# Performance work log

Hardware: AMD Instinct MI355X
Metric: run time of the kernel (lower is better)

Reference implementation:

```python
import jax, jax.numpy as jnp
import numpy as np

B, L, H, R = 8, 128, 768, 24


def setup_inputs() -> dict:
    key = jax.random.key(0)
    ks = jax.random.split(key, 12)
    s = 0.02  # init scale
    f32 = jnp.float32
    inp = {
        "embed_tokens": jax.random.normal(ks[0], (B, L, H), f32),
        "attention_mask": jnp.ones((B, L), f32),
        "target_rel": jax.random.randint(ks[1], (B,), 0, R),
        # relation-judgement head
        "W_hr": jax.random.normal(ks[2], (H, H // 2), f32) * s,
        "b_hr": jnp.zeros((H // 2,), f32),
        "W_rj": jax.random.normal(ks[3], (H // 2, R), f32) * s,
        "b_rj": jnp.zeros((R,), f32),
        # relation embedding
        "rel_emb": jax.random.normal(ks[4], (R, H), f32) * s,
        # correspondence matrix head (input is concat -> 2H)
        "W_corr": jax.random.normal(ks[5], (2 * H, H), f32) * s,
        "b_corr": jnp.zeros((H,), f32),
        "W_gc": jax.random.normal(ks[6], (H, 1), f32) * s,
        "b_gc": jnp.zeros((1,), f32),
        # subject tagging head (fusion_type='concat' -> 2H in, H hidden)
        "W_sh": jax.random.normal(ks[7], (2 * H, H), f32) * s,
        "b_sh": jnp.zeros((H,), f32),
        "W_st": jax.random.normal(ks[8], (H, 3), f32) * s,
        "b_st": jnp.zeros((3,), f32),
        # object tagging head
        "W_oh": jax.random.normal(ks[9], (2 * H, H), f32) * s,
        "b_oh": jnp.zeros((H,), f32),
        "W_ot": jax.random.normal(ks[10], (H, 3), f32) * s,
        "b_ot": jnp.zeros((3,), f32),
    }
    return inp


def reference(embed_tokens, attention_mask, target_rel,
              W_hr, b_hr, W_rj, b_rj, rel_emb,
              W_corr, b_corr, W_gc, b_gc,
              W_sh, b_sh, W_st, b_st,
              W_oh, b_oh, W_ot, b_ot):
    # ---- stage 1: masked mean-pool + relation judgement (dropout = identity at inference)
    masked = embed_tokens * attention_mask[:, :, None]            # [B,L,H]
    pool = jnp.sum(masked, axis=1) / jnp.sum(attention_mask, axis=1)[:, None]  # [B,H]
    rel_hidden = jax.nn.relu(pool @ W_hr + b_hr)                  # [B,H/2]
    stage1 = rel_hidden @ W_rj + b_rj                             # [B,R]

    # ---- correspondence matrix: concat[b,i,j] = [embed[b,j], embed[b,i]]
    # Decompose concat-linear: concat @ W_corr = embed_j @ W1 + embed_i @ W2
    W1, W2 = W_corr[:H_dim(embed_tokens)], W_corr[H_dim(embed_tokens):]
    A = embed_tokens @ W1                                         # [B,L,H] (j-index part)
    C = embed_tokens @ W2                                         # [B,L,H] (i-index part)
    corres_hidden = jax.nn.relu(A[:, None, :, :] + C[:, :, None, :] + b_corr)  # [B,L,L,H]
    pred_corres = corres_hidden @ W_gc + b_gc                     # [B,L,L,1]

    # ---- relation-fused tagging (mode == 'train')
    re = rel_emb[target_rel]                                      # [B,H]
    Bsz, Lsz, Hsz = embed_tokens.shape
    fusion = jnp.concatenate(
        [jnp.broadcast_to(re[:, None, :], (Bsz, Lsz, Hsz)), embed_tokens], axis=-1)  # [B,L,2H]
    subj = jax.nn.relu(fusion @ W_sh + b_sh) @ W_st + b_st        # [B,L,3]
    obj = jax.nn.relu(fusion @ W_oh + b_oh) @ W_ot + b_ot         # [B,L,3]

    return stage1, subj, obj, pred_corres


def H_dim(x):
    return x.shape[-1]
```

## Files before the change

kernel.cpp:

```cpp
#include <hip/hip_runtime.h>
#include <hip/hip_bf16.h>

#define BD   8
#define LD   128
#define HD   768
#define RD   24
#define H2D  384
#define NF   1536
#define WSZ  589824

typedef __attribute__((ext_vector_type(8))) short bf16x8;
typedef __attribute__((ext_vector_type(4))) float f32x4;

__device__ __forceinline__ short f2bf(float f) {
    __hip_bfloat16 h = __float2bfloat16(f);
    return *reinterpret_cast<short*>(&h);
}

__device__ __forceinline__ f32x4 vmax0(f32x4 v) {
    f32x4 r;
    r[0] = fmaxf(v[0], 0.f); r[1] = fmaxf(v[1], 0.f);
    r[2] = fmaxf(v[2], 0.f); r[3] = fmaxf(v[3], 0.f);
    return r;
}

__global__ __launch_bounds__(256) void prep_kernel(
        const float* __restrict__ embed, const float* __restrict__ mask,
        const float* __restrict__ rel_emb, const int* __restrict__ trel,
        const float* __restrict__ W_corr,
        const float* __restrict__ W_sh, const float* __restrict__ b_sh,
        const float* __restrict__ W_oh, const float* __restrict__ b_oh,
        const float* __restrict__ b_st, const float* __restrict__ b_ot,
        float* __restrict__ pool, float* __restrict__ biasrel,
        unsigned short* __restrict__ embedB, unsigned short* __restrict__ WT,
        float* __restrict__ out_subj, float* __restrict__ out_obj) {
    const int q = blockIdx.x, tid = threadIdx.x;

    if (q < 96) {
        const int b = q / 12, c = q % 12;
        __shared__ float mrow[LD];
        __shared__ float msum;
        __shared__ float part[4][64];
        if (tid < LD) mrow[tid] = mask[b * LD + tid];
        __syncthreads();
        if (tid == 0) {
            float s = 0.f;
            for (int l = 0; l < LD; ++l) s += mrow[l];
            msum = s;
        }
        __syncthreads();
        const int lc = tid >> 6, hh = tid & 63;
        const int h = c * 64 + hh;
        float acc = 0.f;
        const float* base = embed + ((size_t)b * LD + lc * 32) * HD + h;
#pragma unroll 8
        for (int i = 0; i < 32; ++i) acc += base[(size_t)i * HD] * mrow[lc * 32 + i];
        part[lc][hh] = acc;
        __syncthreads();
        if (lc == 0)
            pool[b * HD + h] = (part[0][hh] + part[1][hh] + part[2][hh] + part[3][hh]) / msum;
    } else if (q < 192) {
        const int qq = q - 96;
        const int b = qq / 12, cc = qq % 12;
        __shared__ float re[HD];
        __shared__ float part2[2][128];
        const int rel = trel[b];
        for (int k = tid; k < HD; k += 256) re[k] = rel_emb[(size_t)rel * HD + k];
        if (cc == 0 && tid < 3 * LD) {
            const int l = tid / 3, t = tid - 3 * l;
            out_subj[(b * LD + l) * 3 + t] = b_st[t];
            out_obj [(b * LD + l) * 3 + t] = b_ot[t];
        }
        __syncthreads();
        const int kc = tid >> 7, nn = tid & 127;
        const int n = cc * 128 + nn;
        const float* Wp; float bb; int col;
        if (n < HD) { Wp = W_sh; bb = b_sh[n];      col = n; }
        else        { Wp = W_oh; bb = b_oh[n - HD]; col = n - HD; }
        float acc = 0.f;
#pragma unroll 8
        for (int i = 0; i < 384; ++i) {
            const int k = kc * 384 + i;
            acc += re[k] * Wp[(size_t)k * HD + col];
        }
        part2[kc][nn] = acc;
        __syncthreads();
        if (kc == 0) biasrel[b * NF + n] = part2[0][nn] + part2[1][nn] + bb;
    } else if (q < 288) {
        const int base = (q - 192) * 8192;
#pragma unroll
        for (int it = 0; it < 4; ++it) {
            const int off = base + it * 2048 + tid * 8;
            float4 v0 = *(const float4*)&embed[off];
            float4 v1 = *(const float4*)&embed[off + 4];
            bf16x8 p;
            p[0] = f2bf(v0.x); p[1] = f2bf(v0.y); p[2] = f2bf(v0.z); p[3] = f2bf(v0.w);
            p[4] = f2bf(v1.x); p[5] = f2bf(v1.y); p[6] = f2bf(v1.z); p[7] = f2bf(v1.w);
            *(bf16x8*)&embedB[off] = p;
        }
    } else {
        const int qq = q - 288;
        const int w = qq / 144, t = qq % 144;
        const int kt = t / 12, nt = t % 12;
        const float* src = (w == 0) ? W_corr
                         : (w == 1) ? W_corr + WSZ
                         : (w == 2) ? W_sh + WSZ
                                    : W_oh + WSZ;
        unsigned short* dst = WT + (size_t)w * WSZ;
        __shared__ float tile[64 * 65];
        const int r = tid >> 2, c4 = (tid & 3) * 16;
#pragma unroll
        for (int i = 0; i < 4; ++i) {
            float4 v = *(const float4*)&src[(size_t)(kt * 64 + r) * HD + nt * 64 + c4 + i * 4];
            tile[r * 65 + c4 + i * 4 + 0] = v.x;
            tile[r * 65 + c4 + i * 4 + 1] = v.y;
            tile[r * 65 + c4 + i * 4 + 2] = v.z;
            tile[r * 65 + c4 + i * 4 + 3] = v.w;
        }
        __syncthreads();
        bf16x8 p0, p1;
#pragma unroll
        for (int j = 0; j < 8; ++j) {
            p0[j] = f2bf(tile[(c4 + j) * 65 + r]);
            p1[j] = f2bf(tile[(c4 + 8 + j) * 65 + r]);
        }
        unsigned short* o = dst + (size_t)(nt * 64 + r) * HD + kt * 64 + c4;
        *(bf16x8*)(o)     = p0;
        *(bf16x8*)(o + 8) = p1;
    }
}

__global__ __launch_bounds__(256) void biggemm(
        const unsigned short* __restrict__ embedB,
        const unsigned short* __restrict__ WT,
        const float* __restrict__ biasrel,
        const float* __restrict__ W_st, const float* __restrict__ W_ot,
        const float* __restrict__ pool,
        const float* __restrict__ W_hr, const float* __restrict__ b_hr,
        float* __restrict__ AC, float* __restrict__ out_subj,
        float* __restrict__ out_obj, float* __restrict__ rh) {
    const int tid = threadIdx.x;

    if (blockIdx.x >= 24) {
        const int b = blockIdx.y >> 1;
        const int c = (blockIdx.x - 24) * 2 + (blockIdx.y & 1);
        __shared__ float prow[HD];
        __shared__ float rpart[4][64];
        for (int k = tid; k < HD; k += 256) prow[k] = pool[b * HD + k];
        __syncthreads();
        const int kc = tid >> 6, nn = tid & 63;
        const int n = c * 64 + nn;
        float acc = 0.f;
#pragma unroll 8
        for (int i = 0; i < 192; ++i) {
            const int k = kc * 192 + i;
            acc += prow[k] * W_hr[(size_t)k * H2D + n];
        }
        rpart[kc][nn] = acc;
        __syncthreads();
        if (kc == 0)
            rh[b * H2D + n] = fmaxf(rpart[0][nn] + rpart[1][nn] + rpart[2][nn] + rpart[3][nn] + b_hr[n], 0.f);
        return;
    }

    __shared__ __align__(16) short As [64][40];
    __shared__ __align__(16) short Bs0[64][40];
    __shared__ __align__(16) short Bs1[64][40];
    __shared__ float partial[64][3];

    const int bn0 = blockIdx.x * 64;
    const int bm0 = blockIdx.y * 64;

    const unsigned short* W0 = (bn0 < HD) ? WT : WT + WSZ;
    const unsigned short* W1 = (bn0 < HD) ? WT + 2 * (size_t)WSZ : WT + 3 * (size_t)WSZ;
    const int col0 = (bn0 < HD) ? bn0 : bn0 - HD;

    if (tid < 192) partial[tid / 3][tid % 3] = 0.f;

    const int row = tid >> 2;
    const int kc8 = (tid & 3) * 8;
    const int lane = tid & 63;
    const int wv = tid >> 6;
    const int wm = (wv >> 1) * 32;
    const int wn = (wv & 1) * 32;
    const int fr = lane & 15;
    const int kq = (lane >> 4) * 8;
    const int mq = (lane >> 4) * 4;

    f32x4 c00 = {0.f,0.f,0.f,0.f}, c01 = c00, c10 = c00, c11 = c00;
    f32x4 h00 = c00, h01 = c00, h10 = c00, h11 = c00;

    for (int kt = 0; kt < 24; ++kt) {
        const int k0 = kt << 5;
        bf16x8 av = *(const bf16x8*)&embedB[(size_t)(bm0 + row) * HD + k0 + kc8];
        bf16x8 b0v = *(const bf16x8*)&W0[(size_t)(col0 + row) * HD + k0 + kc8];
        bf16x8 b1v = *(const bf16x8*)&W1[(size_t)(col0 + row) * HD + k0 + kc8];

        __syncthreads();
        *(bf16x8*)&As [row][kc8] = av;
        *(bf16x8*)&Bs0[row][kc8] = b0v;
        *(bf16x8*)&Bs1[row][kc8] = b1v;
        __syncthreads();

        bf16x8 a0 = *(bf16x8*)&As[wm + fr][kq];
        bf16x8 a1 = *(bf16x8*)&As[wm + 16 + fr][kq];
        bf16x8 b0 = *(bf16x8*)&Bs0[wn + fr][kq];
        bf16x8 b1 = *(bf16x8*)&Bs0[wn + 16 + fr][kq];
        bf16x8 d0 = *(bf16x8*)&Bs1[wn + fr][kq];
        bf16x8 d1 = *(bf16x8*)&Bs1[wn + 16 + fr][kq];
        c00 = __builtin_amdgcn_mfma_f32_16x16x32_bf16(a0, b0, c00, 0, 0, 0);
        c01 = __builtin_amdgcn_mfma_f32_16x16x32_bf16(a0, b1, c01, 0, 0, 0);
        c10 = __builtin_amdgcn_mfma_f32_16x16x32_bf16(a1, b0, c10, 0, 0, 0);
        c11 = __builtin_amdgcn_mfma_f32_16x16x32_bf16(a1, b1, c11, 0, 0, 0);
        h00 = __builtin_amdgcn_mfma_f32_16x16x32_bf16(a0, d0, h00, 0, 0, 0);
        h01 = __builtin_amdgcn_mfma_f32_16x16x32_bf16(a0, d1, h01, 0, 0, 0);
        h10 = __builtin_amdgcn_mfma_f32_16x16x32_bf16(a1, d0, h10, 0, 0, 0);
        h11 = __builtin_amdgcn_mfma_f32_16x16x32_bf16(a1, d1, h11, 0, 0, 0);
    }

#pragma unroll
    for (int i = 0; i < 2; ++i) {
#pragma unroll
        for (int j = 0; j < 2; ++j) {
            f32x4 a = (i == 0) ? (j == 0 ? c00 : c01) : (j == 0 ? c10 : c11);
            const int ncol = bn0 + wn + j * 16 + fr;
#pragma unroll
            for (int r = 0; r < 4; ++r) {
                const int mrow = bm0 + wm + i * 16 + mq + r;
                AC[(size_t)mrow * NF + ncol] = a[r];
            }
        }
    }

    {
        const float* brl = biasrel + (size_t)(bm0 / LD) * NF;
        const float* Wt = (bn0 < HD) ? W_st : W_ot;
        float* op = (bn0 < HD) ? out_subj : out_obj;
        float pt[8][3] = {};
#pragma unroll
        for (int j = 0; j < 2; ++j) {
            const int ncol = bn0 + wn + j * 16 + fr;
            const int ncl = (bn0 < HD) ? ncol : ncol - HD;
            const float wt0 = Wt[ncl * 3 + 0];
            const float wt1 = Wt[ncl * 3 + 1];
            const float wt2 = Wt[ncl * 3 + 2];
            const float bias = brl[ncol];
#pragma unroll
            for (int i = 0; i < 2; ++i) {
                f32x4 a = (i == 0) ? (j == 0 ? h00 : h01) : (j == 0 ? h10 : h11);
#pragma unroll
                for (int r = 0; r < 4; ++r) {
                    const float v = fmaxf(a[r] + bias, 0.f);
                    pt[i * 4 + r][0] += v * wt0;
                    pt[i * 4 + r][1] += v * wt1;
                    pt[i * 4 + r][2] += v * wt2;
                }
            }
        }
#pragma unroll
        for (int mask = 1; mask < 16; mask <<= 1) {
#pragma unroll
            for (int x = 0; x < 8; ++x)
#pragma unroll
                for (int t = 0; t < 3; ++t)
                    pt[x][t] += __shfl_xor(pt[x][t], mask, 64);
        }
        if (fr == 0) {
#pragma unroll
            for (int i = 0; i < 2; ++i)
#pragma unroll
                for (int r = 0; r < 4; ++r)
#pragma unroll
                    for (int t = 0; t < 3; ++t)
                        atomicAdd(&partial[wm + i * 16 + mq + r][t], pt[i * 4 + r][t]);
        }
        __syncthreads();
        if (tid < 192) {
            const int m = tid / 3, t = tid % 3;
            atomicAdd(&op[(size_t)(bm0 + m) * 3 + t], partial[m][t]);
        }
    }
}

__global__ __launch_bounds__(512) void corres_kernel(
        const float* __restrict__ AC,
        const float* __restrict__ b_corr, const float* __restrict__ W_gc,
        const float* __restrict__ b_gc,
        const float* __restrict__ rh,
        const float* __restrict__ W_rj, const float* __restrict__ b_rj,
        float* __restrict__ out, float* __restrict__ out_stage1) {
    const int b = blockIdx.y;
    const int tid = threadIdx.x;

    if (blockIdx.x == 32) {
        __shared__ float rl[H2D];
        __shared__ float spart[8][RD];
        if (tid < H2D) rl[tid] = rh[b * H2D + tid];
        __syncthreads();
        if (tid < 8 * RD) {
            const int n = tid % RD, kc = tid / RD;
            float acc = 0.f;
#pragma unroll 8
            for (int i = 0; i < 48; ++i) {
                const int k = kc * 48 + i;
                acc += rl[k] * W_rj[k * RD + n];
            }
            spart[kc][n] = acc;
        }
        __syncthreads();
        if (tid < RD) {
            float s = b_rj[tid];
#pragma unroll
            for (int q = 0; q < 8; ++q) s += spart[q][tid];
            out_stage1[b * RD + tid] = s;
        }
        return;
    }

    const int i0 = blockIdx.x * 4;
    const int lane = tid & 63;
    const int wave = tid >> 6;

    f32x4 wg[3], cb[4][3];
#pragma unroll
    for (int s = 0; s < 3; ++s) {
        const int h = s * 256 + lane * 4;
        f32x4 w  = *(const f32x4*)&W_gc[h];
        f32x4 bc = *(const f32x4*)&b_corr[h];
        wg[s] = w;
#pragma unroll
        for (int i = 0; i < 4; ++i) {
            f32x4 cv = *(const f32x4*)&AC[((size_t)(b * LD + i0 + i)) * NF + HD + h];
            cb[i][s] = cv + bc;
        }
    }
    const float bg = b_gc[0];

    f32x4 a[3];
    {
        const float* ar = AC + ((size_t)(b * LD + wave)) * NF;
#pragma unroll
        for (int s = 0; s < 3; ++s) a[s] = *(const f32x4*)&ar[s * 256 + lane * 4];
    }
    for (int j = wave; j < LD; j += 8) {
        f32x4 an[3];
        if (j + 8 < LD) {
            const float* ar = AC + ((size_t)(b * LD + j + 8)) * NF;
#pragma unroll
            for (int s = 0; s < 3; ++s) an[s] = *(const f32x4*)&ar[s * 256 + lane * 4];
        }
        f32x4 sv[4];
#pragma unroll
        for (int i = 0; i < 4; ++i) sv[i] = (f32x4){0.f, 0.f, 0.f, 0.f};
#pragma unroll
        for (int s = 0; s < 3; ++s) {
#pragma unroll
            for (int i = 0; i < 4; ++i)
                sv[i] += vmax0(a[s] + cb[i][s]) * wg[s];
        }
#pragma unroll
        for (int i = 0; i < 4; ++i) {
            float r = (sv[i][0] + sv[i][1]) + (sv[i][2] + sv[i][3]);
#pragma unroll
            for (int off = 32; off > 0; off >>= 1) r += __shfl_down(r, off, 64);
            if (lane == 0)
                out[((size_t)(b * LD + i0 + i)) * LD + j] = r + bg;
        }
#pragma unroll
        for (int s = 0; s < 3; ++s) a[s] = an[s];
    }
}

extern "C" void kernel_launch(void* const* d_in, const int* in_sizes, int n_in,
                              void* d_out, int out_size, void* d_ws, size_t ws_size,
                              hipStream_t stream) {
    const float* embed   = (const float*)d_in[0];
    const float* mask    = (const float*)d_in[1];
    const int*   trel    = (const int*)d_in[2];
    const float* W_hr    = (const float*)d_in[3];
    const float* b_hr    = (const float*)d_in[4];
    const float* W_rj    = (const float*)d_in[5];
    const float* b_rj    = (const float*)d_in[6];
    const float* rel_emb = (const float*)d_in[7];
    const float* W_corr  = (const float*)d_in[8];
    const float* b_corr  = (const float*)d_in[9];
    const float* W_gc    = (const float*)d_in[10];
    const float* b_gc    = (const float*)d_in[11];
    const float* W_sh    = (const float*)d_in[12];
    const float* b_sh    = (const float*)d_in[13];
    const float* W_st    = (const float*)d_in[14];
    const float* b_st    = (const float*)d_in[15];
    const float* W_oh    = (const float*)d_in[16];
    const float* b_oh    = (const float*)d_in[17];
    const float* W_ot    = (const float*)d_in[18];
    const float* b_ot    = (const float*)d_in[19];
    float* out = (float*)d_out;

    float* ws      = (float*)d_ws;
    float* AC      = ws;
    float* biasrel = ws + 1572864;
    float* rh      = ws + 1572864 + 12288;
    float* pool    = ws + 1572864 + 12288 + 3072;
    unsigned short* embedB = (unsigned short*)(ws + 1594368);
    unsigned short* WT     = (unsigned short*)(ws + 1594368 + 393216);

    float* out_stage1 = out;
    float* out_subj   = out + 192;
    float* out_obj    = out + 3264;
    float* out_corr   = out + 6336;

    prep_kernel<<<864, 256, 0, stream>>>(embed, mask, rel_emb, trel, W_corr,
                                         W_sh, b_sh, W_oh, b_oh, b_st, b_ot,
                                         pool, biasrel, embedB, WT,
                                         out_subj, out_obj);

    biggemm<<<dim3(27, 16), 256, 0, stream>>>(embedB, WT, biasrel, W_st, W_ot,
                                              pool, W_hr, b_hr,
                                              AC, out_subj, out_obj, rh);

    corres_kernel<<<dim3(33, BD), 512, 0, stream>>>(AC, b_corr, W_gc, b_gc,
                                                    rh, W_rj, b_rj, out_corr, out_stage1);
}
```

Before: 165.9 us.

## Batch rel-bias matvec across batch and double GEMM K-tile depth

The relation-bias precompute in the prep kernel now handles all 8 batch rows per block. Each weight element is loaded once and reused for 8 batches, so the weight is streamed from global memory once instead of eight times, and the block count drops from 96 to 24. The biggemm main loop now uses a 64-deep K tile with padded LDS rows, which halves the number of barrier-separated iterations. The cost is more shared memory and registers per block, which can reduce occupancy.

```diff
diff --git a/kernel.cpp b/kernel.cpp
--- a/kernel.cpp
+++ b/kernel.cpp
@@ -59,35 +59,48 @@
         __syncthreads();
         if (lc == 0)
             pool[b * HD + h] = (part[0][hh] + part[1][hh] + part[2][hh] + part[3][hh]) / msum;
-    } else if (q < 192) {
-        const int qq = q - 96;
-        const int b = qq / 12, cc = qq % 12;
-        __shared__ float re[HD];
-        __shared__ float part2[2][128];
-        const int rel = trel[b];
-        for (int k = tid; k < HD; k += 256) re[k] = rel_emb[(size_t)rel * HD + k];
-        if (cc == 0 && tid < 3 * LD) {
-            const int l = tid / 3, t = tid - 3 * l;
-            out_subj[(b * LD + l) * 3 + t] = b_st[t];
-            out_obj [(b * LD + l) * 3 + t] = b_ot[t];
-        }
-        __syncthreads();
-        const int kc = tid >> 7, nn = tid & 127;
-        const int n = cc * 128 + nn;
-        const float* Wp; float bb; int col;
-        if (n < HD) { Wp = W_sh; bb = b_sh[n];      col = n; }
-        else        { Wp = W_oh; bb = b_oh[n - HD]; col = n - HD; }
-        float acc = 0.f;
-#pragma unroll 8
-        for (int i = 0; i < 384; ++i) {
-            const int k = kc * 384 + i;
-            acc += re[k] * Wp[(size_t)k * HD + col];
-        }
-        part2[kc][nn] = acc;
-        __syncthreads();
-        if (kc == 0) biasrel[b * NF + n] = part2[0][nn] + part2[1][nn] + bb;
-    } else if (q < 288) {
-        const int base = (q - 192) * 8192;
+    } else if (q < 120) {
+        const int c = q - 96;
+        __shared__ float reAll[8][HD];
+        __shared__ float part[4][8][64];
+        for (int u = tid; u < 8 * HD; u += 256) {
+            const int b = u / HD, k = u - b * HD;
+            reAll[b][k] = rel_emb[(size_t)trel[b] * HD + k];
+        }
+        if (c == 0) {
+            for (int u = tid; u < 3 * LD * BD; u += 256) {
+                const int b = u / (3 * LD), rem = u - b * (3 * LD);
+                const int l = rem / 3, t = rem - 3 * l;
+                out_subj[(b * LD + l) * 3 + t] = b_st[t];
+                out_obj [(b * LD + l) * 3 + t] = b_ot[t];
+            }
+        }
+        __syncthreads();
+        const int kc = tid >> 6, nn = tid & 63;
+        const int n = c * 64 + nn;
+        const float* Wp; int col;
+        if (n < HD) { Wp = W_sh; col = n; }
+        else        { Wp = W_oh; col = n - HD; }
+        float acc[8] = {};
+        for (int i = 0; i < 192; ++i) {
+            const int k = kc * 192 + i;
+            const float w = Wp[(size_t)k * HD + col];
+#pragma unroll
+            for (int b = 0; b < 8; ++b) acc[b] += reAll[b][k] * w;
+        }
+#pragma unroll
+        for (int b = 0; b < 8; ++b) part[kc][b][nn] = acc[b];
+        __syncthreads();
+        {
+            const float bb = (n < HD) ? b_sh[col] : b_oh[col];
+            const int b0 = kc, b1 = kc + 4;
+            float s0 = part[0][b0][nn] + part[1][b0][nn] + part[2][b0][nn] + part[3][b0][nn];
+            float s1 = part[0][b1][nn] + part[1][b1][nn] + part[2][b1][nn] + part[3][b1][nn];
+            biasrel[b0 * NF + n] = s0 + bb;
+            biasrel[b1 * NF + n] = s1 + bb;
+        }
+    } else if (q < 216) {
+        const int base = (q - 120) * 8192;
 #pragma unroll
         for (int it = 0; it < 4; ++it) {
             const int off = base + it * 2048 + tid * 8;
@@ -99,7 +112,7 @@
             *(bf16x8*)&embedB[off] = p;
         }
     } else {
-        const int qq = q - 288;
+        const int qq = q - 216;
         const int w = qq / 144, t = qq % 144;
         const int kt = t / 12, nt = t % 12;
         const float* src = (w == 0) ? W_corr
@@ -163,9 +176,9 @@
         return;
     }
 
-    __shared__ __align__(16) short As [64][40];
-    __shared__ __align__(16) short Bs0[64][40];
-    __shared__ __align__(16) short Bs1[64][40];
+    __shared__ __align__(16) short As [64][76];
+    __shared__ __align__(16) short Bs0[64][76];
+    __shared__ __align__(16) short Bs1[64][76];
     __shared__ float partial[64][3];
 
     const int bn0 = blockIdx.x * 64;
@@ -179,6 +192,7 @@
 
     const int row = tid >> 2;
     const int kc8 = (tid & 3) * 8;
+
     const int lane = tid & 63;
     const int wv = tid >> 6;
     const int wm = (wv >> 1) * 32;
@@ -190,32 +204,44 @@
     f32x4 c00 = {0.f,0.f,0.f,0.f}, c01 = c00, c10 = c00, c11 = c00;
     f32x4 h00 = c00, h01 = c00, h10 = c00, h11 = c00;
 
-    for (int kt = 0; kt < 24; ++kt) {
-        const int k0 = kt << 5;
-        bf16x8 av = *(const bf16x8*)&embedB[(size_t)(bm0 + row) * HD + k0 + kc8];
-        bf16x8 b0v = *(const bf16x8*)&W0[(size_t)(col0 + row) * HD + k0 + kc8];
-        bf16x8 b1v = *(const bf16x8*)&W1[(size_t)(col0 + row) * HD + k0 + kc8];
-
-        __syncthreads();
-        *(bf16x8*)&As [row][kc8] = av;
-        *(bf16x8*)&Bs0[row][kc8] = b0v;
-        *(bf16x8*)&Bs1[row][kc8] = b1v;
-        __syncthreads();
-
-        bf16x8 a0 = *(bf16x8*)&As[wm + fr][kq];
-        bf16x8 a1 = *(bf16x8*)&As[wm + 16 + fr][kq];
-        bf16x8 b0 = *(bf16x8*)&Bs0[wn + fr][kq];
-        bf16x8 b1 = *(bf16x8*)&Bs0[wn + 16 + fr][kq];
-        bf16x8 d0 = *(bf16x8*)&Bs1[wn + fr][kq];
-        bf16x8 d1 = *(bf16x8*)&Bs1[wn + 16 + fr][kq];
-        c00 = __builtin_amdgcn_mfma_f32_16x16x32_bf16(a0, b0, c00, 0, 0, 0);
-        c01 = __builtin_amdgcn_mfma_f32_16x16x32_bf16(a0, b1, c01, 0, 0, 0);
-        c10 = __builtin_amdgcn_mfma_f32_16x16x32_bf16(a1, b0, c10, 0, 0, 0);
-        c11 = __builtin_amdgcn_mfma_f32_16x16x32_bf16(a1, b1, c11, 0, 0, 0);
-        h00 = __builtin_amdgcn_mfma_f32_16x16x32_bf16(a0, d0, h00, 0, 0, 0);
-        h01 = __builtin_amdgcn_mfma_f32_16x16x32_bf16(a0, d1, h01, 0, 0, 0);
-        h10 = __builtin_amdgcn_mfma_f32_16x16x32_bf16(a1, d0, h10, 0, 0, 0);
-        h11 = __builtin_amdgcn_mfma_f32_16x16x32_bf16(a1, d1, h11, 0, 0, 0);
+    for (int kt = 0; kt < 12; ++kt) {
+        const int k0 = kt << 6;
+        const size_t ea = (size_t)(bm0 + row) * HD + k0 + kc8;
+        const size_t wa = (size_t)(col0 + row) * HD + k0 + kc8;
+        bf16x8 av0 = *(const bf16x8*)&embedB[ea];
+        bf16x8 av1 = *(const bf16x8*)&embedB[ea + 32];
+        bf16x8 b0v0 = *(const bf16x8*)&W0[wa];
+        bf16x8 b0v1 = *(const bf16x8*)&W0[wa + 32];
+        bf16x8 b1v0 = *(const bf16x8*)&W1[wa];
+        bf16x8 b1v1 = *(const bf16x8*)&W1[wa + 32];
+
+        __syncthreads();
+        *(bf16x8*)&As [row][kc8]      = av0;
+        *(bf16x8*)&As [row][kc8 + 32] = av1;
+        *(bf16x8*)&Bs0[row][kc8]      = b0v0;
+        *(bf16x8*)&Bs0[row][kc8 + 32] = b0v1;
+        *(bf16x8*)&Bs1[row][kc8]      = b1v0;
+        *(bf16x8*)&Bs1[row][kc8 + 32] = b1v1;
+        __syncthreads();
+
+#pragma unroll
+        for (int kk = 0; kk < 2; ++kk) {
+            const int kx = kq + kk * 32;
+            bf16x8 a0 = *(bf16x8*)&As[wm + fr][kx];
+            bf16x8 a1 = *(bf16x8*)&As[wm + 16 + fr][kx];
+            bf16x8 b0 = *(bf16x8*)&Bs0[wn + fr][kx];
+            bf16x8 b1 = *(bf16x8*)&Bs0[wn + 16 + fr][kx];
+            bf16x8 d0 = *(bf16x8*)&Bs1[wn + fr][kx];
+            bf16x8 d1 = *(bf16x8*)&Bs1[wn + 16 + fr][kx];
+            c00 = __builtin_amdgcn_mfma_f32_16x16x32_bf16(a0, b0, c00, 0, 0, 0);
+            c01 = __builtin_amdgcn_mfma_f32_16x16x32_bf16(a0, b1, c01, 0, 0, 0);
+            c10 = __builtin_amdgcn_mfma_f32_16x16x32_bf16(a1, b0, c10, 0, 0, 0);
+            c11 = __builtin_amdgcn_mfma_f32_16x16x32_bf16(a1, b1, c11, 0, 0, 0);
+            h00 = __builtin_amdgcn_mfma_f32_16x16x32_bf16(a0, d0, h00, 0, 0, 0);
+            h01 = __builtin_amdgcn_mfma_f32_16x16x32_bf16(a0, d1, h01, 0, 0, 0);
+            h10 = __builtin_amdgcn_mfma_f32_16x16x32_bf16(a1, d0, h10, 0, 0, 0);
+            h11 = __builtin_amdgcn_mfma_f32_16x16x32_bf16(a1, d1, h11, 0, 0, 0);
+        }
     }
 
 #pragma unroll
@@ -409,7 +435,7 @@
     float* out_obj    = out + 3264;
     float* out_corr   = out + 6336;
 
-    prep_kernel<<<864, 256, 0, stream>>>(embed, mask, rel_emb, trel, W_corr,
+    prep_kernel<<<792, 256, 0, stream>>>(embed, mask, rel_emb, trel, W_corr,
                                          W_sh, b_sh, W_oh, b_oh, b_st, b_ot,
                                          pool, biasrel, embedB, WT,
                                          out_subj, out_obj);
```

Result: faster. 160.9 us (-3.0%).
